# Kernel optimization log

Measured on AMD Instinct MI355X. Metric: run time of the kernel, lower is better.

## Reference

```python
import jax, jax.numpy as jnp
import numpy as np

LENGTH = 4000
N_PAD = 4096  # smallest power of 2 >= LENGTH


def _hadamard(n: int) -> jnp.ndarray:
    """Sylvester-construction Hadamard matrix (matches scipy.linalg.hadamard)."""
    H = np.array([[1.0]], dtype=np.float32)
    while H.shape[0] < n:
        H = np.block([[H, H], [H, -H]])
    return jnp.asarray(H, dtype=jnp.float32)


def setup_inputs() -> dict:
    key = jax.random.key(0)
    k1, k2, k3, k4 = jax.random.split(key, 4)
    x = jax.random.normal(k1, (8, 64, LENGTH), dtype=jnp.float32)          # [B, Cin, L]
    W = jax.random.normal(k2, (4, 64, 64), dtype=jnp.float32) * 0.1       # [P, Cout, Cin] (1x1 conv, no bias)
    T = jax.random.uniform(k3, (4, N_PAD), dtype=jnp.float32) / 10.0      # per-pod soft thresholds
    v = jax.random.uniform(k4, (4, N_PAD), dtype=jnp.float32)             # per-pod spectral scale
    return {"x": x, "W": W, "T": T, "v": v}


def reference(x, W, T, v):
    H = _hadamard(N_PAD)                                                  # [n, n], symmetric
    # zero-pad to power of two
    f0 = jnp.pad(x, ((0, 0), (0, 0), (0, N_PAD - LENGTH)))                # [B, Cin, n]
    # forward WHT along last axis: u @ H
    f1 = f0 @ H                                                           # [B, Cin, n]
    # per-pod: v_i * f1 -> 1x1 conv -> soft-threshold
    z = v[:, None, None, :] * f1[None]                                    # [P, B, Cin, n]
    c = jnp.einsum('poi,pbin->pbon', W, z)                                # [P, B, Cout, n]
    st = jnp.sign(c) * jax.nn.relu(jnp.abs(c) - jnp.abs(T)[:, None, None, :])
    f6 = st.sum(axis=0)                                                   # [B, Cout, n]
    # inverse WHT: u @ H / n, then crop
    y = (f6 @ H) * (1.0 / N_PAD)
    y = y[..., :LENGTH]
    return y + x  # residual
```

## Files before the change

### kernel.cpp

```cpp
#include <hip/hip_runtime.h>
#include <hip/hip_bf16.h>

#define LENGTH 4000
#define NPAD   4096
#define NB     8
#define CH     64
#define NP     4
#define NT2    32
#define BSTR   72

using ushort8 = __attribute__((ext_vector_type(8))) unsigned short;
using short8v = __attribute__((ext_vector_type(8))) short;
using f32x4   = __attribute__((ext_vector_type(4))) float;

__device__ __forceinline__ unsigned short f2bu(float f) {
    __hip_bfloat16 h = __float2bfloat16(f);
    return __builtin_bit_cast(unsigned short, h);
}
__device__ __forceinline__ float bu2f(unsigned short u) {
    __hip_bfloat16 h = __builtin_bit_cast(__hip_bfloat16, u);
    return __bfloat162float(h);
}

__device__ __forceinline__ void fwht16(float v[16]) {
    #pragma unroll
    for (int h = 1; h < 16; h <<= 1)
        #pragma unroll
        for (int j = 0; j < 16; j += 2 * h)
            #pragma unroll
            for (int k = j; k < j + h; ++k) {
                float u = v[k], w = v[k + h];
                v[k] = u + w; v[k + h] = u - w;
            }
}

__global__ __launch_bounds__(256) void k_fwht_fwd(const float* __restrict__ x,
                                                  unsigned short* __restrict__ f1b,
                                                  const float* __restrict__ W,
                                                  unsigned short* __restrict__ Wb) {
    __shared__ float lds[256 * 17];
    const int row = blockIdx.x;
    const int t = threadIdx.x;
    const int A = t >> 4, B = t & 15;

    if (row < NP * CH && t < CH)
        Wb[row * CH + t] = f2bu(W[row * CH + t]);

    float v[16];
    if (t < 250) {
        const float* xr = x + (size_t)row * LENGTH + t * 16;
        #pragma unroll
        for (int q = 0; q < 4; ++q) {
            float4 lv = *(const float4*)(xr + q * 4);
            v[q * 4 + 0] = lv.x; v[q * 4 + 1] = lv.y;
            v[q * 4 + 2] = lv.z; v[q * 4 + 3] = lv.w;
        }
    } else {
        #pragma unroll
        for (int c = 0; c < 16; ++c) v[c] = 0.f;
    }
    fwht16(v);

    #pragma unroll
    for (int c = 0; c < 16; ++c)
        lds[(A * 16 + c) * 17 + B] = v[c];
    __syncthreads();
    {
        const int base = (A * 16 + B) * 17;
        #pragma unroll
        for (int b = 0; b < 16; ++b) v[b] = lds[base + b];
    }
    __syncthreads();
    fwht16(v);

    const int C = t & 15;
    #pragma unroll
    for (int b = 0; b < 16; ++b)
        lds[(b * 16 + C) * 17 + A] = v[b];
    __syncthreads();
    {
        const int base2 = t * 17;
        #pragma unroll
        for (int a = 0; a < 16; ++a) v[a] = lds[base2 + a];
    }
    fwht16(v);

    unsigned short* fr = f1b + (size_t)row * NPAD;
    #pragma unroll
    for (int a = 0; a < 16; ++a)
        fr[a * 256 + t] = f2bu(v[a]);
}

__global__ __launch_bounds__(256) void k_mix(const unsigned short* __restrict__ f1b,
                                             const unsigned short* __restrict__ Wb,
                                             const float* __restrict__ T,
                                             const float* __restrict__ v,
                                             unsigned short* __restrict__ f6b) {
    __shared__ unsigned short sBt[NT2 * BSTR];
    const int bid = blockIdx.x;
    const int nchunk = bid & 127;
    const int b = bid >> 7;
    const int nbase = nchunk * NT2;
    const int t = threadIdx.x;
    const int lane = t & 63;
    const int w = t >> 6;
    const int l15 = lane & 15, lq = lane >> 4;

    {
        const int i = t >> 2, n0 = (t & 3) * 8;
        const unsigned short* src =
            f1b + (size_t)(b * CH + i) * NPAD + nbase + n0;
        ushort8 r = *(const ushort8*)src;
        #pragma unroll
        for (int j = 0; j < 8; ++j)
            sBt[(n0 + j) * BSTR + i] = r[j];
    }

    short8v afrag[NP][2];
    #pragma unroll
    for (int p = 0; p < NP; ++p)
        #pragma unroll
        for (int ks = 0; ks < 2; ++ks)
            afrag[p][ks] = *(const short8v*)(Wb +
                (size_t)(p * 64 + w * 16 + l15) * CH + ks * 32 + lq * 8);

    __syncthreads();

    short8v bfrag[2][2];
    #pragma unroll
    for (int nt = 0; nt < 2; ++nt)
        #pragma unroll
        for (int ks = 0; ks < 2; ++ks)
            bfrag[nt][ks] = *(const short8v*)(
                &sBt[(nt * 16 + l15) * BSTR + ks * 32 + lq * 8]);

    f32x4 acc[NP][2];
    #pragma unroll
    for (int p = 0; p < NP; ++p)
        #pragma unroll
        for (int nt = 0; nt < 2; ++nt) {
            acc[p][nt] = (f32x4){0.f, 0.f, 0.f, 0.f};
            #pragma unroll
            for (int ks = 0; ks < 2; ++ks)
                acc[p][nt] = __builtin_amdgcn_mfma_f32_16x16x32_bf16(
                    afrag[p][ks], bfrag[nt][ks], acc[p][nt], 0, 0, 0);
        }

    #pragma unroll
    for (int nt = 0; nt < 2; ++nt) {
        const int n = nbase + nt * 16 + l15;
        float outv[4] = {0.f, 0.f, 0.f, 0.f};
        #pragma unroll
        for (int p = 0; p < NP; ++p) {
            const float vp = v[(size_t)p * NPAD + n];
            const float tp = fabsf(T[(size_t)p * NPAD + n]);
            #pragma unroll
            for (int r = 0; r < 4; ++r) {
                float c = vp * acc[p][nt][r];
                float a = fabsf(c) - tp;
                outv[r] += (a > 0.f) ? copysignf(a, c) : 0.f;
            }
        }
        #pragma unroll
        for (int r = 0; r < 4; ++r) {
            const int o = w * 16 + lq * 4 + r;
            f6b[(size_t)(b * CH + o) * NPAD + n] = f2bu(outv[r]);
        }
    }
}

__global__ __launch_bounds__(256) void k_fwht_inv(const unsigned short* __restrict__ f6b,
                                                  const float* __restrict__ x,
                                                  float* __restrict__ out) {
    __shared__ float lds[256 * 17];
    const int row = blockIdx.x;
    const int t = threadIdx.x;
    const int A = t >> 4, B = t & 15;

    float v[16];
    {
        const unsigned short* fr = f6b + (size_t)row * NPAD + t * 16;
        ushort8 r0 = *(const ushort8*)(fr);
        ushort8 r1 = *(const ushort8*)(fr + 8);
        #pragma unroll
        for (int j = 0; j < 8; ++j) { v[j] = bu2f(r0[j]); v[8 + j] = bu2f(r1[j]); }
    }
    fwht16(v);

    #pragma unroll
    for (int c = 0; c < 16; ++c)
        lds[(A * 16 + c) * 17 + B] = v[c];
    __syncthreads();
    {
        const int base = (A * 16 + B) * 17;
        #pragma unroll
        for (int b = 0; b < 16; ++b) v[b] = lds[base + b];
    }
    __syncthreads();
    fwht16(v);

    const int C = t & 15;
    #pragma unroll
    for (int b = 0; b < 16; ++b)
        lds[(b * 16 + C) * 17 + A] = v[b];
    __syncthreads();
    {
        const int base2 = t * 17;
        #pragma unroll
        for (int a = 0; a < 16; ++a) v[a] = lds[base2 + a];
    }
    fwht16(v);

    const float scale = 1.f / NPAD;
    const float* xr = x + (size_t)row * LENGTH;
    float* orow = out + (size_t)row * LENGTH;
    #pragma unroll
    for (int a = 0; a < 16; ++a) {
        int n = a * 256 + t;
        if (n < LENGTH) orow[n] = v[a] * scale + xr[n];
    }
}

extern "C" void kernel_launch(void* const* d_in, const int* in_sizes, int n_in,
                              void* d_out, int out_size, void* d_ws, size_t ws_size,
                              hipStream_t stream) {
    (void)in_sizes; (void)n_in; (void)out_size; (void)ws_size;
    const float* x = (const float*)d_in[0];
    const float* W = (const float*)d_in[1];
    const float* T = (const float*)d_in[2];
    const float* v = (const float*)d_in[3];
    float* out = (float*)d_out;
    unsigned short* f1b = (unsigned short*)d_ws;
    unsigned short* f6b = f1b + (size_t)NB * CH * NPAD;
    unsigned short* Wb  = f6b + (size_t)NB * CH * NPAD;

    k_fwht_fwd<<<NB * CH, 256, 0, stream>>>(x, f1b, W, Wb);
    k_mix<<<NB * (NPAD / NT2), 256, 0, stream>>>(f1b, Wb, T, v, f6b);
    k_fwht_inv<<<NB * CH, 256, 0, stream>>>(f6b, x, out);
}
```

Before: 23.56 us.

## Restructure FWHT kernels to radix-8 with 512 threads per row

Both the forward and inverse Walsh-Hadamard kernels move from 256 threads doing three radix-16 butterfly passes to 512 threads doing four radix-8 passes. Exchanges go through two ping-ponged LDS buffers with a padded address mapping, which lets one __syncthreads per stage be dropped. The aim is more parallelism and fewer registers per thread, for better latency hiding. The cost is an extra LDS exchange round and more total LDS traffic.

```diff
diff --git a/kernel.cpp b/kernel.cpp
--- a/kernel.cpp
+++ b/kernel.cpp
@@ -22,73 +22,72 @@
     return __bfloat162float(h);
 }
 
-__device__ __forceinline__ void fwht16(float v[16]) {
-    #pragma unroll
-    for (int h = 1; h < 16; h <<= 1)
-        #pragma unroll
-        for (int j = 0; j < 16; j += 2 * h)
+__device__ __forceinline__ void fwht8(float v[8]) {
+    #pragma unroll
+    for (int h = 1; h < 8; h <<= 1)
+        #pragma unroll
+        for (int j = 0; j < 8; j += 2 * h)
             #pragma unroll
             for (int k = j; k < j + h; ++k) {
-                float u = v[k], w = v[k + h];
-                v[k] = u + w; v[k + h] = u - w;
+                float a = v[k], b = v[k + h];
+                v[k] = a + b; v[k + h] = a - b;
             }
 }
 
-__global__ __launch_bounds__(256) void k_fwht_fwd(const float* __restrict__ x,
+#define LADR(n) ((((n) >> 3) * 9) + ((n) & 7))
+#define LDSZ 4608
+
+__global__ __launch_bounds__(512) void k_fwht_fwd(const float* __restrict__ x,
                                                   unsigned short* __restrict__ f1b,
                                                   const float* __restrict__ W,
                                                   unsigned short* __restrict__ Wb) {
-    __shared__ float lds[256 * 17];
+    __shared__ float ldsA[LDSZ];
+    __shared__ float ldsB[LDSZ];
     const int row = blockIdx.x;
     const int t = threadIdx.x;
-    const int A = t >> 4, B = t & 15;
 
     if (row < NP * CH && t < CH)
         Wb[row * CH + t] = f2bu(W[row * CH + t]);
 
-    float v[16];
-    if (t < 250) {
-        const float* xr = x + (size_t)row * LENGTH + t * 16;
-        #pragma unroll
-        for (int q = 0; q < 4; ++q) {
-            float4 lv = *(const float4*)(xr + q * 4);
-            v[q * 4 + 0] = lv.x; v[q * 4 + 1] = lv.y;
-            v[q * 4 + 2] = lv.z; v[q * 4 + 3] = lv.w;
-        }
+    float v[8];
+    if (t < 500) {
+        const float* xr = x + (size_t)row * LENGTH + t * 8;
+        float4 a = *(const float4*)xr, b = *(const float4*)(xr + 4);
+        v[0]=a.x; v[1]=a.y; v[2]=a.z; v[3]=a.w;
+        v[4]=b.x; v[5]=b.y; v[6]=b.z; v[7]=b.w;
     } else {
         #pragma unroll
-        for (int c = 0; c < 16; ++c) v[c] = 0.f;
-    }
-    fwht16(v);
-
-    #pragma unroll
-    for (int c = 0; c < 16; ++c)
-        lds[(A * 16 + c) * 17 + B] = v[c];
-    __syncthreads();
-    {
-        const int base = (A * 16 + B) * 17;
-        #pragma unroll
-        for (int b = 0; b < 16; ++b) v[b] = lds[base + b];
-    }
-    __syncthreads();
-    fwht16(v);
-
-    const int C = t & 15;
-    #pragma unroll
-    for (int b = 0; b < 16; ++b)
-        lds[(b * 16 + C) * 17 + A] = v[b];
-    __syncthreads();
-    {
-        const int base2 = t * 17;
-        #pragma unroll
-        for (int a = 0; a < 16; ++a) v[a] = lds[base2 + a];
-    }
-    fwht16(v);
+        for (int j = 0; j < 8; ++j) v[j] = 0.f;
+    }
+    fwht8(v);
+
+    #pragma unroll
+    for (int j = 0; j < 8; ++j) ldsA[LADR(t * 8 + j)] = v[j];
+    __syncthreads();
+    const int s1 = (t >> 3) * 64 + (t & 7);
+    #pragma unroll
+    for (int j = 0; j < 8; ++j) v[j] = ldsA[LADR(s1 + j * 8)];
+    fwht8(v);
+
+    #pragma unroll
+    for (int j = 0; j < 8; ++j) ldsB[LADR(s1 + j * 8)] = v[j];
+    __syncthreads();
+    const int s2 = (t >> 6) * 512 + ((t >> 3) & 7) * 8 + (t & 7);
+    #pragma unroll
+    for (int j = 0; j < 8; ++j) v[j] = ldsB[LADR(s2 + j * 64)];
+    fwht8(v);
+
+    #pragma unroll
+    for (int j = 0; j < 8; ++j) ldsA[LADR(s2 + j * 64)] = v[j];
+    __syncthreads();
+    #pragma unroll
+    for (int j = 0; j < 8; ++j) v[j] = ldsA[LADR(j * 512 + t)];
+    fwht8(v);
 
     unsigned short* fr = f1b + (size_t)row * NPAD;
     #pragma unroll
-    for (int a = 0; a < 16; ++a)
-        fr[a * 256 + t] = f2bu(v[a]);
+    for (int j = 0; j < 8; ++j)
+        fr[j * 512 + t] = f2bu(v[j]);
 }
 
 __global__ __launch_bounds__(256) void k_mix(const unsigned short* __restrict__ f1b,
@@ -169,55 +168,53 @@
     }
 }
 
-__global__ __launch_bounds__(256) void k_fwht_inv(const unsigned short* __restrict__ f6b,
+__global__ __launch_bounds__(512) void k_fwht_inv(const unsigned short* __restrict__ f6b,
                                                   const float* __restrict__ x,
                                                   float* __restrict__ out) {
-    __shared__ float lds[256 * 17];
+    __shared__ float ldsA[LDSZ];
+    __shared__ float ldsB[LDSZ];
     const int row = blockIdx.x;
     const int t = threadIdx.x;
-    const int A = t >> 4, B = t & 15;
-
-    float v[16];
+
+    float v[8];
     {
-        const unsigned short* fr = f6b + (size_t)row * NPAD + t * 16;
-        ushort8 r0 = *(const ushort8*)(fr);
-        ushort8 r1 = *(const ushort8*)(fr + 8);
-        #pragma unroll
-        for (int j = 0; j < 8; ++j) { v[j] = bu2f(r0[j]); v[8 + j] = bu2f(r1[j]); }
-    }
-    fwht16(v);
-
-    #pragma unroll
-    for (int c = 0; c < 16; ++c)
-        lds[(A * 16 + c) * 17 + B] = v[c];
-    __syncthreads();
-    {
-        const int base = (A * 16 + B) * 17;
-        #pragma unroll
-        for (int b = 0; b < 16; ++b) v[b] = lds[base + b];
-    }
-    __syncthreads();
-    fwht16(v);
-
-    const int C = t & 15;
-    #pragma unroll
-    for (int b = 0; b < 16; ++b)
-        lds[(b * 16 + C) * 17 + A] = v[b];
-    __syncthreads();
-    {
-        const int base2 = t * 17;
-        #pragma unroll
-        for (int a = 0; a < 16; ++a) v[a] = lds[base2 + a];
-    }
-    fwht16(v);
+        const unsigned short* fr = f6b + (size_t)row * NPAD + t * 8;
+        ushort8 r = *(const ushort8*)fr;
+        #pragma unroll
+        for (int j = 0; j < 8; ++j) v[j] = bu2f(r[j]);
+    }
+    fwht8(v);
+
+    #pragma unroll
+    for (int j = 0; j < 8; ++j) ldsA[LADR(t * 8 + j)] = v[j];
+    __syncthreads();
+    const int s1 = (t >> 3) * 64 + (t & 7);
+    #pragma unroll
+    for (int j = 0; j < 8; ++j) v[j] = ldsA[LADR(s1 + j * 8)];
+    fwht8(v);
+
+    #pragma unroll
+    for (int j = 0; j < 8; ++j) ldsB[LADR(s1 + j * 8)] = v[j];
+    __syncthreads();
+    const int s2 = (t >> 6) * 512 + ((t >> 3) & 7) * 8 + (t & 7);
+    #pragma unroll
+    for (int j = 0; j < 8; ++j) v[j] = ldsB[LADR(s2 + j * 64)];
+    fwht8(v);
+
+    #pragma unroll
+    for (int j = 0; j < 8; ++j) ldsA[LADR(s2 + j * 64)] = v[j];
+    __syncthreads();
+    #pragma unroll
+    for (int j = 0; j < 8; ++j) v[j] = ldsA[LADR(j * 512 + t)];
+    fwht8(v);
 
     const float scale = 1.f / NPAD;
     const float* xr = x + (size_t)row * LENGTH;
     float* orow = out + (size_t)row * LENGTH;
     #pragma unroll
-    for (int a = 0; a < 16; ++a) {
-        int n = a * 256 + t;
-        if (n < LENGTH) orow[n] = v[a] * scale + xr[n];
+    for (int j = 0; j < 8; ++j) {
+        const int n = j * 512 + t;
+        if (n < LENGTH) orow[n] = v[j] * scale + xr[n];
     }
 }
 
@@ -234,7 +231,7 @@
     unsigned short* f6b = f1b + (size_t)NB * CH * NPAD;
     unsigned short* Wb  = f6b + (size_t)NB * CH * NPAD;
 
-    k_fwht_fwd<<<NB * CH, 256, 0, stream>>>(x, f1b, W, Wb);
+    k_fwht_fwd<<<NB * CH, 512, 0, stream>>>(x, f1b, W, Wb);
     k_mix<<<NB * (NPAD / NT2), 256, 0, stream>>>(f1b, Wb, T, v, f6b);
-    k_fwht_inv<<<NB * CH, 256, 0, stream>>>(f6b, x, out);
-}
+    k_fwht_inv<<<NB * CH, 512, 0, stream>>>(f6b, x, out);
+}
```

New measurement: 23.13 us (median of 2 runs). Within noise of the previous version (-1.8%).
